# Optimization experiments

Measured on AMD Instinct MI355X. Metric: run time of the kernel, lower is better.

## Reference

```python
import jax, jax.numpy as jnp
import numpy as np
import math

B, S, D, H = 4, 2048, 1024, 16
DH = D // H  # 64


def setup_inputs() -> dict:
    key = jax.random.key(0)
    ks = jax.random.split(key, 7)
    scale = 1.0 / math.sqrt(D)
    q = jax.random.normal(ks[0], (B, S, D), dtype=jnp.float32)
    k = jax.random.normal(ks[1], (B, S, D), dtype=jnp.float32)
    v = jax.random.normal(ks[2], (B, S, D), dtype=jnp.float32)
    mask = jnp.tril(jnp.ones((S, S), dtype=jnp.int32))[None, None]  # [1,1,S,S] causal
    wq = jax.random.normal(ks[3], (D, D), dtype=jnp.float32) * scale
    wk = jax.random.normal(ks[4], (D, D), dtype=jnp.float32) * scale
    wv = jax.random.normal(ks[5], (D, D), dtype=jnp.float32) * scale
    wo = jax.random.normal(ks[6], (D, D), dtype=jnp.float32) * scale
    return {"q": q, "k": k, "v": v, "mask": mask, "wq": wq, "wk": wk, "wv": wv, "wo": wo}


def reference(q, k, v, mask, wq, wk, wv, wo):
    # nn.Linear(bias=False): y = x @ W.T
    qry = q @ wq.T
    key = k @ wk.T
    val = v @ wv.T
    # [B,S,D] -> [B,H,S,DH]
    qry = qry.reshape(B, S, H, DH).transpose(0, 2, 1, 3)
    key = key.reshape(B, S, H, DH).transpose(0, 2, 1, 3)
    val = val.reshape(B, S, H, DH).transpose(0, 2, 1, 3)
    scores = jnp.einsum('bhqd,bhkd->bhqk', qry, key) / math.sqrt(DH)
    scores = jnp.where(mask == 0, jnp.float32(-1e9), scores)
    attn = jax.nn.softmax(scores, axis=-1)  # dropout p=0.0 -> identity
    x = jnp.einsum('bhqk,bhkd->bhqd', attn, val)
    x = x.transpose(0, 2, 1, 3).reshape(B, S, D)
    return x @ wo.T
```

## Files before the change

### kernel.cpp

```cpp
#include <hip/hip_runtime.h>
#include <hip/hip_bf16.h>

typedef __attribute__((ext_vector_type(8))) short bf16x8;
typedef __attribute__((ext_vector_type(4))) float f32x4;
typedef __attribute__((ext_vector_type(16))) float f32x16;

#define MFMA16(a, b, c) __builtin_amdgcn_mfma_f32_16x16x32_bf16((a), (b), (c), 0, 0, 0)
#define MFMA32(a, b, c) __builtin_amdgcn_mfma_f32_32x32x16_bf16((a), (b), (c), 0, 0, 0)

#if defined(__has_builtin)
#if __has_builtin(__builtin_amdgcn_exp2f)
#define EXP2(x) __builtin_amdgcn_exp2f(x)
#endif
#endif
#ifndef EXP2
#define EXP2(x) exp2f(x)
#endif

__device__ __forceinline__ short f2b(float f) {
  unsigned u = __builtin_bit_cast(unsigned, f);
  u += 0x7FFFu + ((u >> 16) & 1u);
  return (short)(u >> 16);
}
__device__ __forceinline__ unsigned cvtpk(float lo, float hi) {
  unsigned r;
  asm("v_cvt_pk_bf16_f32 %0, %1, %2" : "=v"(r) : "v"(lo), "v"(hi));
  return r;
}
__device__ __forceinline__ bf16x8 cvt8(float4 a, float4 b) {
  bf16x8 o;
  o[0] = f2b(a.x); o[1] = f2b(a.y); o[2] = f2b(a.z); o[3] = f2b(a.w);
  o[4] = f2b(b.x); o[5] = f2b(b.y); o[6] = f2b(b.z); o[7] = f2b(b.w);
  return o;
}

__global__ __launch_bounds__(256) void cvt4_bf16(const float* __restrict__ s0,
                                                 const float* __restrict__ s1,
                                                 const float* __restrict__ s2,
                                                 const float* __restrict__ s3,
                                                 short* __restrict__ d, long stride) {
  const int which = blockIdx.y;
  const float* s = which == 0 ? s0 : (which == 1 ? s1 : (which == 2 ? s2 : s3));
  long i = (long)blockIdx.x * 256 + threadIdx.x;
  const float4* sp = (const float4*)s;
  *(bf16x8*)(d + which * stride + i * 8) = cvt8(sp[2 * i], sp[2 * i + 1]);
}

template <int MODE>
__global__ __launch_bounds__(256) void gemm_proj(const float* __restrict__ A_,
                                                 const short* __restrict__ BT_,
                                                 short* __restrict__ Cout,
                                                 float oscale) {
  __shared__ __align__(16) short As[128 * 64];
  __shared__ __align__(16) short Bs[128 * 64];
  const int t = threadIdx.x;
  const int l = t & 63, w = t >> 6;
  const int grp = l >> 4, li = l & 15;
  const int wg = (((int)blockIdx.x & 7) << 6) | ((int)blockIdx.x >> 3);
  const int bm = wg >> 3, bn = wg & 7;
  const int m0 = bm << 7, n0 = bn << 7;
  const int wm = (w >> 1) << 6, wn = (w & 1) << 6;
  const int srow = t >> 3, scol = (t & 7) << 3;
  f32x4 acc[4][4] = {};

  float4 pa[4][2];
  bf16x8 pb[4];
#define PLOAD(KT)                                                            \
  {                                                                          \
    _Pragma("unroll") for (int i = 0; i < 4; ++i) {                          \
      const float* ga = A_ + (long)(m0 + i * 32 + srow) * 1024 + (KT) * 64 + scol; \
      pa[i][0] = *(const float4*)ga;                                         \
      pa[i][1] = *(const float4*)(ga + 4);                                   \
      pb[i] = *(const bf16x8*)(BT_ + (long)(n0 + i * 32 + srow) * 1024 + (KT) * 64 + scol); \
    }                                                                        \
  }
#define PWRITE()                                                             \
  {                                                                          \
    _Pragma("unroll") for (int i = 0; i < 4; ++i) {                          \
      *(bf16x8*)&As[i * 2048 + t * 8] = cvt8(pa[i][0], pa[i][1]);            \
      *(bf16x8*)&Bs[i * 2048 + t * 8] = pb[i];                               \
    }                                                                        \
  }

  PLOAD(0);
  PWRITE();
  __syncthreads();
#pragma unroll 1
  for (int kt = 0; kt < 16; ++kt) {
    if (kt + 1 < 16) PLOAD(kt + 1);
#pragma unroll
    for (int kk = 0; kk < 64; kk += 32) {
      bf16x8 af[4], bfr[4];
#pragma unroll
      for (int mi = 0; mi < 4; ++mi)
        af[mi] = *(const bf16x8*)&As[(wm + mi * 16 + li) * 64 + kk + grp * 8];
#pragma unroll
      for (int ni = 0; ni < 4; ++ni)
        bfr[ni] = *(const bf16x8*)&Bs[(wn + ni * 16 + li) * 64 + kk + grp * 8];
#pragma unroll
      for (int mi = 0; mi < 4; ++mi)
#pragma unroll
        for (int ni = 0; ni < 4; ++ni)
          acc[mi][ni] = MFMA16(af[mi], bfr[ni], acc[mi][ni]);
    }
    __syncthreads();
    if (kt + 1 < 16) {
      PWRITE();
      __syncthreads();
    }
  }
#undef PLOAD
#undef PWRITE
#pragma unroll
  for (int mi = 0; mi < 4; ++mi) {
#pragma unroll
    for (int ni = 0; ni < 4; ++ni) {
      f32x4 v = acc[mi][ni];
      int n = n0 + wn + ni * 16 + li;
#pragma unroll
      for (int r = 0; r < 4; ++r) {
        int m = m0 + wm + mi * 16 + grp * 4 + r;
        int b = m >> 11, sq = m & 2047;
        int h = n >> 6, dh = n & 63;
        if (MODE == 0)
          Cout[(((long)(b * 16 + h) * 2048 + sq) << 6) + dh] = f2b(v[r] * oscale);
        else
          Cout[(((long)(b * 16 + h) * 64 + dh) << 11) + sq] = f2b(v[r]);
      }
    }
  }
}

__global__ __launch_bounds__(256) void gemm_out(const short* __restrict__ A_,
                                                const short* __restrict__ BT_,
                                                float* __restrict__ Cout) {
  __shared__ __align__(16) short As[128 * 64];
  __shared__ __align__(16) short Bs[128 * 64];
  const int t = threadIdx.x;
  const int l = t & 63, w = t >> 6;
  const int grp = l >> 4, li = l & 15;
  const int wg = (((int)blockIdx.x & 7) << 6) | ((int)blockIdx.x >> 3);
  const int bm = wg >> 3, bn = wg & 7;
  const int m0 = bm << 7, n0 = bn << 7;
  const int wm = (w >> 1) << 6, wn = (w & 1) << 6;
  const int srow = t >> 3, scol = (t & 7) << 3;
  f32x4 acc[4][4] = {};
#pragma unroll 1
  for (int kt = 0; kt < 16; ++kt) {
#pragma unroll
    for (int i = 0; i < 4; ++i) {
      const short* ga = A_ + (long)(m0 + i * 32 + srow) * 1024 + kt * 64 + scol;
      __builtin_amdgcn_global_load_lds(
          (const __attribute__((address_space(1))) void*)ga,
          (__attribute__((address_space(3))) void*)&As[i * 2048 + t * 8], 16, 0, 0);
      const short* gb = BT_ + (long)(n0 + i * 32 + srow) * 1024 + kt * 64 + scol;
      __builtin_amdgcn_global_load_lds(
          (const __attribute__((address_space(1))) void*)gb,
          (__attribute__((address_space(3))) void*)&Bs[i * 2048 + t * 8], 16, 0, 0);
    }
    __syncthreads();
#pragma unroll
    for (int kk = 0; kk < 64; kk += 32) {
      bf16x8 af[4], bfr[4];
#pragma unroll
      for (int mi = 0; mi < 4; ++mi)
        af[mi] = *(const bf16x8*)&As[(wm + mi * 16 + li) * 64 + kk + grp * 8];
#pragma unroll
      for (int ni = 0; ni < 4; ++ni)
        bfr[ni] = *(const bf16x8*)&Bs[(wn + ni * 16 + li) * 64 + kk + grp * 8];
#pragma unroll
      for (int mi = 0; mi < 4; ++mi)
#pragma unroll
        for (int ni = 0; ni < 4; ++ni)
          acc[mi][ni] = MFMA16(af[mi], bfr[ni], acc[mi][ni]);
    }
    __syncthreads();
  }
#pragma unroll
  for (int mi = 0; mi < 4; ++mi) {
#pragma unroll
    for (int ni = 0; ni < 4; ++ni) {
      f32x4 v = acc[mi][ni];
      int n = n0 + wn + ni * 16 + li;
#pragma unroll
      for (int r = 0; r < 4; ++r) {
        int m = m0 + wm + mi * 16 + grp * 4 + r;
        Cout[(long)m * 1024 + n] = v[r];
      }
    }
  }
}

__device__ __forceinline__ void attn_tile(const short* Kbuf, const short* Vbuf,
                                          const bf16x8 qf[4], f32x16& oa, f32x16& ob,
                                          float& mrun, float& lsum, int kt, bool diag,
                                          int khmax, int qg, int q, int hi) {
  f32x16 p0 = {}, p1 = {};
  __builtin_amdgcn_s_setprio(1);
#pragma unroll
  for (int kd = 0; kd < 4; ++kd) {
    int colB = kd * 32 + hi * 16;
    bf16x8 kf0 = *(const bf16x8*)((const char*)Kbuf + q * 128 + (colB ^ ((q & 7) << 4)));
    p0 = MFMA32(kf0, qf[kd], p0);
  }
  if (khmax == 2) {
#pragma unroll
    for (int kd = 0; kd < 4; ++kd) {
      int colB = kd * 32 + hi * 16;
      bf16x8 kf1 = *(const bf16x8*)((const char*)Kbuf + (q + 32) * 128 + (colB ^ ((q & 7) << 4)));
      p1 = MFMA32(kf1, qf[kd], p1);
    }
  }
  __builtin_amdgcn_s_setprio(0);
  if (diag) {
#pragma unroll
    for (int r = 0; r < 16; ++r) {
      int key0 = kt * 64 + (r & 3) + 8 * (r >> 2) + 4 * hi;
      if (key0 > qg) p0[r] = -1e30f;
      if (key0 + 32 > qg) p1[r] = -1e30f;
    }
  }
  float pm = p0[0];
#pragma unroll
  for (int r = 1; r < 16; ++r) pm = fmaxf(pm, p0[r]);
  if (khmax == 2) {
#pragma unroll
    for (int r = 0; r < 16; ++r) pm = fmaxf(pm, p1[r]);
  }
  pm = fmaxf(pm, __shfl_xor(pm, 32));
  const bool skip = __all(pm - mrun <= 11.5f);
  float mn;
  float alpha = 1.f;
  if (skip) {
    mn = mrun;
  } else {
    mn = fmaxf(mrun, pm);
    alpha = EXP2(mrun - mn);
    mrun = mn;
  }
  float ts = 0.f;
#pragma unroll
  for (int r = 0; r < 16; ++r) { p0[r] = EXP2(p0[r] - mn); ts += p0[r]; }
  if (khmax == 2) {
#pragma unroll
    for (int r = 0; r < 16; ++r) { p1[r] = EXP2(p1[r] - mn); ts += p1[r]; }
  }
  ts += __shfl_xor(ts, 32);
  if (skip) {
    lsum += ts;
  } else {
    lsum = lsum * alpha + ts;
#pragma unroll
    for (int r = 0; r < 16; ++r) { oa[r] *= alpha; ob[r] *= alpha; }
  }
  unsigned own0[8], prt0[8], own1[8], prt1[8];
#pragma unroll
  for (int g = 0; g < 4; ++g) {
    own0[2 * g]     = cvtpk(p0[4 * g], p0[4 * g + 1]);
    own0[2 * g + 1] = cvtpk(p0[4 * g + 2], p0[4 * g + 3]);
  }
#pragma unroll
  for (int i = 0; i < 8; ++i) prt0[i] = __shfl_xor(own0[i], 32);
  if (khmax == 2) {
#pragma unroll
    for (int g = 0; g < 4; ++g) {
      own1[2 * g]     = cvtpk(p1[4 * g], p1[4 * g + 1]);
      own1[2 * g + 1] = cvtpk(p1[4 * g + 2], p1[4 * g + 3]);
    }
#pragma unroll
    for (int i = 0; i < 8; ++i) prt1[i] = __shfl_xor(own1[i], 32);
  }
  __builtin_amdgcn_s_setprio(1);
#define PVSTEP(KD, OWN, PRT)                                                              \
  {                                                                                       \
    const int kdl = (KD) & 1;                                                             \
    unsigned b0 = hi ? PRT[4 * kdl + 2] : OWN[4 * kdl];                                   \
    unsigned b1 = hi ? PRT[4 * kdl + 3] : OWN[4 * kdl + 1];                               \
    unsigned b2 = hi ? OWN[4 * kdl + 2] : PRT[4 * kdl];                                   \
    unsigned b3 = hi ? OWN[4 * kdl + 3] : PRT[4 * kdl + 1];                               \
    int4 bi = {(int)b0, (int)b1, (int)b2, (int)b3};                                       \
    bf16x8 pb = __builtin_bit_cast(bf16x8, bi);                                           \
    int colB = (KD) * 32 + hi * 16;                                                       \
    bf16x8 vf0 = *(const bf16x8*)((const char*)Vbuf + q * 128 + (colB ^ ((q & 7) << 4))); \
    bf16x8 vf1 = *(const bf16x8*)((const char*)Vbuf + (q + 32) * 128 + (colB ^ ((q & 7) << 4))); \
    oa = MFMA32(vf0, pb, oa);                                                             \
    ob = MFMA32(vf1, pb, ob);                                                             \
  }
  PVSTEP(0, own0, prt0);
  PVSTEP(1, own0, prt0);
  if (khmax == 2) {
    PVSTEP(2, own1, prt1);
    PVSTEP(3, own1, prt1);
  }
#undef PVSTEP
  __builtin_amdgcn_s_setprio(0);
}

__global__ __launch_bounds__(256, 2) void attn_fwd(const short* __restrict__ Qh,
                                                   const short* __restrict__ Kh,
                                                   const short* __restrict__ Vt,
                                                   short* __restrict__ Xb) {
  __shared__ __align__(16) short Ks[2][4096];
  __shared__ __align__(16) short Vs[2][4096];
  const int bh = blockIdx.x;
  const int qtA = blockIdx.y;
  const int qtB = 15 - qtA;
  const int t = threadIdx.x, l = t & 63, w = t >> 6;
  const int q = l & 31, hi = l >> 5;
  const int q0wA = qtA * 128 + w * 32, q0wB = qtB * 128 + w * 32;
  const int qgA = q0wA + q, qgB = q0wB + q;
  const short* Qp = Qh + (long)bh * 131072;
  const char* Kb = (const char*)(Kh + (long)bh * 131072);
  const char* Vb = (const char*)(Vt + (long)bh * 131072);

  bf16x8 qfA[4], qfB[4];
#pragma unroll
  for (int kd = 0; kd < 4; ++kd) {
    qfA[kd] = *(const bf16x8*)(Qp + (long)qgA * 64 + kd * 16 + hi * 8);
    qfB[kd] = *(const bf16x8*)(Qp + (long)qgB * 64 + kd * 16 + hi * 8);
  }

  const int co0 = t * 16, co1 = co0 + 4096;

  f32x16 oaA = {}, obA = {}, oaB = {}, obB = {};
  float mrunA = -1e30f, lsumA = 0.f, mrunB = -1e30f, lsumB = 0.f;
  const int tripsA = (q0wA >> 6) + 1;
  const int tripsB = (q0wB >> 6) + 1;
  const int nt = 2 * qtB + 2;

#define STAGE(KT, BUF)                                                                   \
  {                                                                                      \
    long ktb = (long)(KT) * 8192;                                                        \
    _Pragma("unroll") for (int c = 0; c < 2; ++c) {                                      \
      int o = c ? co1 : co0;                                                             \
      int ksrc = o ^ (((o >> 7) & 7) << 4);                                              \
      __builtin_amdgcn_global_load_lds(                                                  \
          (const __attribute__((address_space(1))) void*)(Kb + ktb + ksrc),              \
          (__attribute__((address_space(3))) void*)((char*)Ks[BUF] + o), 16, 0, 0);      \
      int row = o >> 7, c16 = (o >> 4) & 7;                                              \
      int vsrc = row * 4096 + (KT) * 128 + (((c16 ^ (row & 7))) << 4);                   \
      __builtin_amdgcn_global_load_lds(                                                  \
          (const __attribute__((address_space(1))) void*)(Vb + vsrc),                    \
          (__attribute__((address_space(3))) void*)((char*)Vs[BUF] + o), 16, 0, 0);      \
    }                                                                                    \
  }

  STAGE(0, 0);
  __syncthreads();

  for (int kt = 0; kt < nt; ++kt) {
    const int buf = kt & 1;
    if (kt + 1 < nt) STAGE(kt + 1, buf ^ 1);

    if (kt < tripsB) {
      const bool diag = (kt == tripsB - 1);
      const int khmax = (diag && ((q0wB & 32) == 0)) ? 1 : 2;
      attn_tile(Ks[buf], Vs[buf], qfB, oaB, obB, mrunB, lsumB, kt, diag, khmax, qgB, q, hi);
    }
    if (kt < tripsA) {
      const bool diag = (kt == tripsA - 1);
      const int khmax = (diag && ((q0wA & 32) == 0)) ? 1 : 2;
      attn_tile(Ks[buf], Vs[buf], qfA, oaA, obA, mrunA, lsumA, kt, diag, khmax, qgA, q, hi);
    }
    __syncthreads();
  }

  const int b = bh >> 4, h = bh & 15;
#define EPI(OA, OB, LS, QG)                                                \
  {                                                                        \
    const float inv = 1.f / (LS);                                          \
    short* orow = Xb + (long)(b * 2048 + (QG)) * 1024 + h * 64;            \
    _Pragma("unroll") for (int g = 0; g < 4; ++g) {                        \
      unsigned u0 = cvtpk((OA)[4 * g] * inv, (OA)[4 * g + 1] * inv);       \
      unsigned u1 = cvtpk((OA)[4 * g + 2] * inv, (OA)[4 * g + 3] * inv);   \
      uint2 uu = {u0, u1};                                                 \
      *(uint2*)(orow + 8 * g + 4 * hi) = uu;                               \
      unsigned w0 = cvtpk((OB)[4 * g] * inv, (OB)[4 * g + 1] * inv);       \
      unsigned w1 = cvtpk((OB)[4 * g + 2] * inv, (OB)[4 * g + 3] * inv);   \
      uint2 ww = {w0, w1};                                                 \
      *(uint2*)(orow + 32 + 8 * g + 4 * hi) = ww;                          \
    }                                                                      \
  }
  EPI(oaA, obA, lsumA, qgA);
  EPI(oaB, obB, lsumB, qgB);
#undef EPI
}

extern "C" void kernel_launch(void* const* d_in, const int* in_sizes, int n_in,
                              void* d_out, int out_size, void* d_ws, size_t ws_size,
                              hipStream_t stream) {
  const float* q  = (const float*)d_in[0];
  const float* k  = (const float*)d_in[1];
  const float* v  = (const float*)d_in[2];
  const float* wq = (const float*)d_in[4];
  const float* wk = (const float*)d_in[5];
  const float* wv = (const float*)d_in[6];
  const float* wo = (const float*)d_in[7];

  short* ws = (short*)d_ws;
  const long T = 8388608;
  short* Qh  = ws;
  short* Kh  = Qh + T;
  short* Vt  = Kh + T;
  short* Xb  = Vt + T;
  short* wqb = Xb + T;
  short* wkb = wqb + 1048576;
  short* wvb = wkb + 1048576;
  short* wob = wvb + 1048576;

  cvt4_bf16<<<dim3(512, 4), 256, 0, stream>>>(wq, wk, wv, wo, wqb, 1048576);

  gemm_proj<0><<<512, 256, 0, stream>>>(q, wqb, Qh, 0.18033688f);
  gemm_proj<0><<<512, 256, 0, stream>>>(k, wkb, Kh, 1.0f);
  gemm_proj<1><<<512, 256, 0, stream>>>(v, wvb, Vt, 1.0f);
  attn_fwd<<<dim3(64, 8), 256, 0, stream>>>(Qh, Kh, Vt, Xb);
  gemm_out<<<512, 256, 0, stream>>>(Xb, wob, (float*)d_out);
}
```

Before: 199.2 us.

## Share K/V fragment loads across both query tiles and interleave their softmax phases

The per-tile helper is inlined into the main loop so that the K and V fragments read from shared memory are loaded once per key tile and reused by both paired query tiles (A and B), instead of being reloaded in each call. The two tiles' QK and softmax phases now run back to back before a combined PV phase, which gives the scheduler more independent work to overlap. In exchange it holds more fragments and packed probabilities in registers at once, which at two waves per SIMD could cause spills or a lower occupancy.

```diff
diff --git a/kernel.cpp b/kernel.cpp
--- a/kernel.cpp
+++ b/kernel.cpp
@@ -191,111 +191,6 @@
   }
 }
 
-__device__ __forceinline__ void attn_tile(const short* Kbuf, const short* Vbuf,
-                                          const bf16x8 qf[4], f32x16& oa, f32x16& ob,
-                                          float& mrun, float& lsum, int kt, bool diag,
-                                          int khmax, int qg, int q, int hi) {
-  f32x16 p0 = {}, p1 = {};
-  __builtin_amdgcn_s_setprio(1);
-#pragma unroll
-  for (int kd = 0; kd < 4; ++kd) {
-    int colB = kd * 32 + hi * 16;
-    bf16x8 kf0 = *(const bf16x8*)((const char*)Kbuf + q * 128 + (colB ^ ((q & 7) << 4)));
-    p0 = MFMA32(kf0, qf[kd], p0);
-  }
-  if (khmax == 2) {
-#pragma unroll
-    for (int kd = 0; kd < 4; ++kd) {
-      int colB = kd * 32 + hi * 16;
-      bf16x8 kf1 = *(const bf16x8*)((const char*)Kbuf + (q + 32) * 128 + (colB ^ ((q & 7) << 4)));
-      p1 = MFMA32(kf1, qf[kd], p1);
-    }
-  }
-  __builtin_amdgcn_s_setprio(0);
-  if (diag) {
-#pragma unroll
-    for (int r = 0; r < 16; ++r) {
-      int key0 = kt * 64 + (r & 3) + 8 * (r >> 2) + 4 * hi;
-      if (key0 > qg) p0[r] = -1e30f;
-      if (key0 + 32 > qg) p1[r] = -1e30f;
-    }
-  }
-  float pm = p0[0];
-#pragma unroll
-  for (int r = 1; r < 16; ++r) pm = fmaxf(pm, p0[r]);
-  if (khmax == 2) {
-#pragma unroll
-    for (int r = 0; r < 16; ++r) pm = fmaxf(pm, p1[r]);
-  }
-  pm = fmaxf(pm, __shfl_xor(pm, 32));
-  const bool skip = __all(pm - mrun <= 11.5f);
-  float mn;
-  float alpha = 1.f;
-  if (skip) {
-    mn = mrun;
-  } else {
-    mn = fmaxf(mrun, pm);
-    alpha = EXP2(mrun - mn);
-    mrun = mn;
-  }
-  float ts = 0.f;
-#pragma unroll
-  for (int r = 0; r < 16; ++r) { p0[r] = EXP2(p0[r] - mn); ts += p0[r]; }
-  if (khmax == 2) {
-#pragma unroll
-    for (int r = 0; r < 16; ++r) { p1[r] = EXP2(p1[r] - mn); ts += p1[r]; }
-  }
-  ts += __shfl_xor(ts, 32);
-  if (skip) {
-    lsum += ts;
-  } else {
-    lsum = lsum * alpha + ts;
-#pragma unroll
-    for (int r = 0; r < 16; ++r) { oa[r] *= alpha; ob[r] *= alpha; }
-  }
-  unsigned own0[8], prt0[8], own1[8], prt1[8];
-#pragma unroll
-  for (int g = 0; g < 4; ++g) {
-    own0[2 * g]     = cvtpk(p0[4 * g], p0[4 * g + 1]);
-    own0[2 * g + 1] = cvtpk(p0[4 * g + 2], p0[4 * g + 3]);
-  }
-#pragma unroll
-  for (int i = 0; i < 8; ++i) prt0[i] = __shfl_xor(own0[i], 32);
-  if (khmax == 2) {
-#pragma unroll
-    for (int g = 0; g < 4; ++g) {
-      own1[2 * g]     = cvtpk(p1[4 * g], p1[4 * g + 1]);
-      own1[2 * g + 1] = cvtpk(p1[4 * g + 2], p1[4 * g + 3]);
-    }
-#pragma unroll
-    for (int i = 0; i < 8; ++i) prt1[i] = __shfl_xor(own1[i], 32);
-  }
-  __builtin_amdgcn_s_setprio(1);
-#define PVSTEP(KD, OWN, PRT)                                                              \
-  {                                                                                       \
-    const int kdl = (KD) & 1;                                                             \
-    unsigned b0 = hi ? PRT[4 * kdl + 2] : OWN[4 * kdl];                                   \
-    unsigned b1 = hi ? PRT[4 * kdl + 3] : OWN[4 * kdl + 1];                               \
-    unsigned b2 = hi ? OWN[4 * kdl + 2] : PRT[4 * kdl];                                   \
-    unsigned b3 = hi ? OWN[4 * kdl + 3] : PRT[4 * kdl + 1];                               \
-    int4 bi = {(int)b0, (int)b1, (int)b2, (int)b3};                                       \
-    bf16x8 pb = __builtin_bit_cast(bf16x8, bi);                                           \
-    int colB = (KD) * 32 + hi * 16;                                                       \
-    bf16x8 vf0 = *(const bf16x8*)((const char*)Vbuf + q * 128 + (colB ^ ((q & 7) << 4))); \
-    bf16x8 vf1 = *(const bf16x8*)((const char*)Vbuf + (q + 32) * 128 + (colB ^ ((q & 7) << 4))); \
-    oa = MFMA32(vf0, pb, oa);                                                             \
-    ob = MFMA32(vf1, pb, ob);                                                             \
-  }
-  PVSTEP(0, own0, prt0);
-  PVSTEP(1, own0, prt0);
-  if (khmax == 2) {
-    PVSTEP(2, own1, prt1);
-    PVSTEP(3, own1, prt1);
-  }
-#undef PVSTEP
-  __builtin_amdgcn_s_setprio(0);
-}
-
 __global__ __launch_bounds__(256, 2) void attn_fwd(const short* __restrict__ Qh,
                                                    const short* __restrict__ Kh,
                                                    const short* __restrict__ Vt,
@@ -352,15 +247,153 @@
     const int buf = kt & 1;
     if (kt + 1 < nt) STAGE(kt + 1, buf ^ 1);
 
-    if (kt < tripsB) {
-      const bool diag = (kt == tripsB - 1);
-      const int khmax = (diag && ((q0wB & 32) == 0)) ? 1 : 2;
-      attn_tile(Ks[buf], Vs[buf], qfB, oaB, obB, mrunB, lsumB, kt, diag, khmax, qgB, q, hi);
-    }
-    if (kt < tripsA) {
-      const bool diag = (kt == tripsA - 1);
-      const int khmax = (diag && ((q0wA & 32) == 0)) ? 1 : 2;
-      attn_tile(Ks[buf], Vs[buf], qfA, oaA, obA, mrunA, lsumA, kt, diag, khmax, qgA, q, hi);
+    const bool doB = (kt < tripsB);
+    const bool doA = (kt < tripsA);
+    if (doB) {
+      const short* Kbuf = Ks[buf];
+      const short* Vbuf = Vs[buf];
+      const bool diagB = (kt == tripsB - 1);
+      const int khB = (diagB && ((q0wB & 32) == 0)) ? 1 : 2;
+      const bool diagA = doA && (kt == tripsA - 1);
+      const int khA = (doA && diagA && ((q0wA & 32) == 0)) ? 1 : 2;
+      const bool needHi = (khB == 2) || (doA && khA == 2);
+
+      bf16x8 kf0[4], kf1[4];
+#pragma unroll
+      for (int kd = 0; kd < 4; ++kd) {
+        int colB = kd * 32 + hi * 16;
+        kf0[kd] = *(const bf16x8*)((const char*)Kbuf + q * 128 + (colB ^ ((q & 7) << 4)));
+      }
+      if (needHi) {
+#pragma unroll
+        for (int kd = 0; kd < 4; ++kd) {
+          int colB = kd * 32 + hi * 16;
+          kf1[kd] = *(const bf16x8*)((const char*)Kbuf + (q + 32) * 128 + (colB ^ ((q & 7) << 4)));
+        }
+      }
+
+      unsigned ownB0[8], prtB0[8], ownB1[8], prtB1[8];
+      unsigned ownA0[8], prtA0[8], ownA1[8], prtA1[8];
+      int khBv = khB, khAv = khA;
+
+#define MEMBER(QF, OA, OB, MRUN, LSUM, DIAG, KHM, QG, OWN0, PRT0, OWN1, PRT1)    \
+      {                                                                          \
+        f32x16 p0 = {}, p1 = {};                                                 \
+        __builtin_amdgcn_s_setprio(1);                                           \
+        _Pragma("unroll") for (int kd = 0; kd < 4; ++kd)                         \
+          p0 = MFMA32(kf0[kd], QF[kd], p0);                                      \
+        if ((KHM) == 2) {                                                        \
+          _Pragma("unroll") for (int kd = 0; kd < 4; ++kd)                       \
+            p1 = MFMA32(kf1[kd], QF[kd], p1);                                    \
+        }                                                                        \
+        __builtin_amdgcn_s_setprio(0);                                           \
+        if (DIAG) {                                                              \
+          _Pragma("unroll") for (int r = 0; r < 16; ++r) {                       \
+            int key0 = kt * 64 + (r & 3) + 8 * (r >> 2) + 4 * hi;                \
+            if (key0 > (QG)) p0[r] = -1e30f;                                     \
+            if (key0 + 32 > (QG)) p1[r] = -1e30f;                                \
+          }                                                                      \
+        }                                                                        \
+        float pm = p0[0];                                                        \
+        _Pragma("unroll") for (int r = 1; r < 16; ++r) pm = fmaxf(pm, p0[r]);    \
+        if ((KHM) == 2) {                                                        \
+          _Pragma("unroll") for (int r = 0; r < 16; ++r) pm = fmaxf(pm, p1[r]);  \
+        }                                                                        \
+        pm = fmaxf(pm, __shfl_xor(pm, 32));                                      \
+        const bool skip = __all(pm - (MRUN) <= 11.5f);                           \
+        float mn;                                                                \
+        float alpha = 1.f;                                                       \
+        if (skip) {                                                              \
+          mn = (MRUN);                                                           \
+        } else {                                                                 \
+          mn = fmaxf((MRUN), pm);                                                \
+          alpha = EXP2((MRUN) - mn);                                             \
+          (MRUN) = mn;                                                           \
+        }                                                                        \
+        float ts = 0.f;                                                          \
+        _Pragma("unroll") for (int r = 0; r < 16; ++r) {                         \
+          p0[r] = EXP2(p0[r] - mn); ts += p0[r];                                 \
+        }                                                                        \
+        if ((KHM) == 2) {                                                        \
+          _Pragma("unroll") for (int r = 0; r < 16; ++r) {                       \
+            p1[r] = EXP2(p1[r] - mn); ts += p1[r];                               \
+          }                                                                      \
+        }                                                                        \
+        ts += __shfl_xor(ts, 32);                                                \
+        if (skip) {                                                              \
+          (LSUM) += ts;                                                          \
+        } else {                                                                 \
+          (LSUM) = (LSUM) * alpha + ts;                                          \
+          _Pragma("unroll") for (int r = 0; r < 16; ++r) {                       \
+            (OA)[r] *= alpha; (OB)[r] *= alpha;                                  \
+          }                                                                      \
+        }                                                                        \
+        _Pragma("unroll") for (int g = 0; g < 4; ++g) {                          \
+          OWN0[2 * g]     = cvtpk(p0[4 * g], p0[4 * g + 1]);                     \
+          OWN0[2 * g + 1] = cvtpk(p0[4 * g + 2], p0[4 * g + 3]);                 \
+        }                                                                        \
+        _Pragma("unroll") for (int i = 0; i < 8; ++i)                            \
+          PRT0[i] = __shfl_xor(OWN0[i], 32);                                     \
+        if ((KHM) == 2) {                                                        \
+          _Pragma("unroll") for (int g = 0; g < 4; ++g) {                        \
+            OWN1[2 * g]     = cvtpk(p1[4 * g], p1[4 * g + 1]);                   \
+            OWN1[2 * g + 1] = cvtpk(p1[4 * g + 2], p1[4 * g + 3]);               \
+          }                                                                      \
+          _Pragma("unroll") for (int i = 0; i < 8; ++i)                          \
+            PRT1[i] = __shfl_xor(OWN1[i], 32);                                   \
+        }                                                                        \
+      }
+
+      MEMBER(qfB, oaB, obB, mrunB, lsumB, diagB, khBv, qgB, ownB0, prtB0, ownB1, prtB1);
+      if (doA)
+        MEMBER(qfA, oaA, obA, mrunA, lsumA, diagA, khAv, qgA, ownA0, prtA0, ownA1, prtA1);
+#undef MEMBER
+
+      bf16x8 vf0[4], vf1[4];
+#pragma unroll
+      for (int kd = 0; kd < 2; ++kd) {
+        int colB = kd * 32 + hi * 16;
+        vf0[kd] = *(const bf16x8*)((const char*)Vbuf + q * 128 + (colB ^ ((q & 7) << 4)));
+        vf1[kd] = *(const bf16x8*)((const char*)Vbuf + (q + 32) * 128 + (colB ^ ((q & 7) << 4)));
+      }
+      if (needHi) {
+#pragma unroll
+        for (int kd = 2; kd < 4; ++kd) {
+          int colB = kd * 32 + hi * 16;
+          vf0[kd] = *(const bf16x8*)((const char*)Vbuf + q * 128 + (colB ^ ((q & 7) << 4)));
+          vf1[kd] = *(const bf16x8*)((const char*)Vbuf + (q + 32) * 128 + (colB ^ ((q & 7) << 4)));
+        }
+      }
+
+      __builtin_amdgcn_s_setprio(1);
+#define PVSTEP(KD, OWN, PRT, OA, OB)                                              \
+      {                                                                           \
+        const int kdl = (KD) & 1;                                                 \
+        unsigned b0 = hi ? PRT[4 * kdl + 2] : OWN[4 * kdl];                       \
+        unsigned b1 = hi ? PRT[4 * kdl + 3] : OWN[4 * kdl + 1];                   \
+        unsigned b2 = hi ? OWN[4 * kdl + 2] : PRT[4 * kdl];                       \
+        unsigned b3 = hi ? OWN[4 * kdl + 3] : PRT[4 * kdl + 1];                   \
+        int4 bi = {(int)b0, (int)b1, (int)b2, (int)b3};                           \
+        bf16x8 pb = __builtin_bit_cast(bf16x8, bi);                               \
+        (OA) = MFMA32(vf0[KD], pb, (OA));                                         \
+        (OB) = MFMA32(vf1[KD], pb, (OB));                                         \
+      }
+      PVSTEP(0, ownB0, prtB0, oaB, obB);
+      PVSTEP(1, ownB0, prtB0, oaB, obB);
+      if (khBv == 2) {
+        PVSTEP(2, ownB1, prtB1, oaB, obB);
+        PVSTEP(3, ownB1, prtB1, oaB, obB);
+      }
+      if (doA) {
+        PVSTEP(0, ownA0, prtA0, oaA, obA);
+        PVSTEP(1, ownA0, prtA0, oaA, obA);
+        if (khAv == 2) {
+          PVSTEP(2, ownA1, prtA1, oaA, obA);
+          PVSTEP(3, ownA1, prtA1, oaA, obA);
+        }
+      }
+#undef PVSTEP
+      __builtin_amdgcn_s_setprio(0);
     }
     __syncthreads();
   }
```

New measurement: 212.0 us. 1.06x slower.
